# Kernel tuning notes

Measured on AMD Instinct MI355X. Metric: run time of the kernel, lower is better.

Reference implementation:

```python
import jax, jax.numpy as jnp
import numpy as np

N = 50000   # nodes
E = 100000  # edges
C = 256     # in_channels


def setup_inputs() -> dict:
    key = jax.random.key(0)
    k1, k2, k3, k4 = jax.random.split(key, 4)
    x = jax.random.normal(k1, (N, C), dtype=jnp.float32)
    edge_index = jax.random.randint(k2, (2, E), 0, N, dtype=jnp.int32)
    # torch nn.Linear default init ~ U(-1/sqrt(C), 1/sqrt(C)); exact dist irrelevant for correctness
    bound = 1.0 / np.sqrt(C)
    W = jax.random.uniform(k3, (C, C), minval=-bound, maxval=bound, dtype=jnp.float32)
    b = jax.random.uniform(k4, (C,), minval=-bound, maxval=bound, dtype=jnp.float32)
    return {"x": x, "edge_index": edge_index, "W": W, "b": b}


def _scatter_mean_with_self_loops(xt, edge_index, n):
    # edge_index_sl = [edges ; self-loops]
    ar = jnp.arange(n, dtype=edge_index.dtype)
    src = jnp.concatenate([edge_index[0], ar])  # [E+N]
    dst = jnp.concatenate([edge_index[1], ar])  # [E+N]
    gathered = xt[src]                           # [E+N, C]
    sums = jax.ops.segment_sum(gathered, dst, num_segments=n)
    cnt = jax.ops.segment_sum(jnp.ones_like(dst, dtype=xt.dtype), dst, num_segments=n)
    # every node has a self-loop so cnt >= 1; guard anyway
    return sums / jnp.maximum(cnt, 1.0)[:, None]


def _merge_edges(edge_index, n):
    # Sequential greedy edge merge, faithful to the Python loop, as a lax.scan.
    remaining0 = jnp.ones((n,), dtype=jnp.int32)
    discarded0 = jnp.zeros((n,), dtype=jnp.int32).at[edge_index[0]].set(1)

    def step(carry, st):
        rem, disc = carry
        s, t = st[0], st[1]
        cond = (rem[s] == 1) & (rem[t] == 1) & (disc[t] == 1) & (s != t)
        rem = rem.at[s].set(jnp.where(cond, 0, rem[s]))
        disc = disc.at[t].set(jnp.where(cond, 0, disc[t]))
        return (rem, disc), None

    (remaining, _), _ = jax.lax.scan(step, (remaining0, discarded0), edge_index.T)
    return remaining  # int32 0/1 mask, 1 = kept node


def reference(x, edge_index, W, b):
    n = x.shape[0]
    xt = x @ W.T + b                                   # self.trans(x)
    h = _scatter_mean_with_self_loops(xt, edge_index, n)  # [N, C]
    mask = _merge_edges(edge_index, n)                 # nodes_remaining
    # Original returns h[mask == 1] (data-dependent shape). For jit-compatibility
    # we return h with dropped rows zeroed, plus the mask; compaction is a
    # trivial post-processing gather.
    out = h * mask.astype(h.dtype)[:, None]
    return out, mask
```

## Files before the change

### kernel.cpp

```cpp
#include <hip/hip_runtime.h>
#include <hip/hip_bf16.h>

#define C_DIM 256

#define MBLK 64
#define MTHR 1024
#define MT_TOT (MBLK * MTHR)
#define MEPT 2
#define EPOCH0 2000u
#define MAXR 1900
#define GROWS 128

typedef __attribute__((ext_vector_type(8))) short bf16x8;
typedef __attribute__((ext_vector_type(4))) float f32x4;

__device__ __forceinline__ unsigned short f32_to_bf16(float f) {
    __hip_bfloat16 h = __float2bfloat16(f);
    return __builtin_bit_cast(unsigned short, h);
}
__device__ __forceinline__ float bf16_to_f32(unsigned short u) {
    unsigned v = ((unsigned)u) << 16;
    return __builtin_bit_cast(float, v);
}
__device__ __forceinline__ unsigned ld_ag(const unsigned* p) {
    return __hip_atomic_load(p, __ATOMIC_RELAXED, __HIP_MEMORY_SCOPE_AGENT);
}
__device__ __forceinline__ unsigned long long ld_ag8(const unsigned* p) {
    return __hip_atomic_load((const unsigned long long*)p, __ATOMIC_RELAXED, __HIP_MEMORY_SCOPE_AGENT);
}

__global__ __launch_bounds__(256) void prep(const float* __restrict__ W,
                                            unsigned short* __restrict__ W_bf,
                                            const int* __restrict__ esrc,
                                            const int* __restrict__ edst,
                                            unsigned char* __restrict__ disc0,
                                            int* __restrict__ cnt,
                                            unsigned short* __restrict__ slots,
                                            int E) {
    int tid = blockIdx.x * blockDim.x + threadIdx.x;
    int T = gridDim.x * blockDim.x;
    for (int i = tid; i < C_DIM * C_DIM; i += T) W_bf[i] = f32_to_bf16(W[i]);
    for (int e = tid; e < E; e += T) {
        int s = esrc[e], t = edst[e];
        disc0[s] = 1;
        int pos = atomicAdd(&cnt[t], 1);
        if (pos < 32) slots[(size_t)t * 32 + pos] = (unsigned short)s;
    }
}

__global__ __launch_bounds__(1024) void fused_kernel(
    const float* __restrict__ X, const unsigned short* __restrict__ W_bf,
    const float* __restrict__ bias, float* __restrict__ out,
    const int* __restrict__ cnt, const unsigned short* __restrict__ slots,
    const int* __restrict__ esrc, const int* __restrict__ edst,
    const unsigned char* __restrict__ disc0,
    unsigned* __restrict__ mins, unsigned* __restrict__ bar,
    float* __restrict__ remf, int E, int N) {
    __shared__ unsigned short Xs[GROWS][264];

    if (blockIdx.x >= MBLK) {
        const int i0 = (int)(blockIdx.x - MBLK) * GROWS;
        const int tid = threadIdx.x;
        const int w = tid >> 6, l = tid & 63;

        for (int nn = 0; nn < 8; ++nn) {
            int lrow = w * 8 + nn;
            int node = i0 + lrow;
            float4 s = make_float4(0.f, 0.f, 0.f, 0.f);
            if (node < N) {
                s = *(const float4*)&X[(size_t)node * C_DIM + l * 4];
                int deg = cnt[node];
                int dl = deg > 32 ? 32 : deg;
                const unsigned short* sl = slots + (size_t)node * 32;
                unsigned long long sl4 = *(const unsigned long long*)sl;
                int dl4 = dl > 4 ? 4 : dl;
#pragma unroll 4
                for (int j = 0; j < dl4; ++j) {
                    int src = (int)((sl4 >> (16 * j)) & 0xFFFFull);
                    float4 v = *(const float4*)&X[(size_t)src * C_DIM + l * 4];
                    s.x += v.x; s.y += v.y; s.z += v.z; s.w += v.w;
                }
                for (int j = 4; j < dl; ++j) {
                    int src = sl[j];
                    float4 v = *(const float4*)&X[(size_t)src * C_DIM + l * 4];
                    s.x += v.x; s.y += v.y; s.z += v.z; s.w += v.w;
                }
                float inv = 1.f / (float)(deg + 1);
                s.x *= inv; s.y *= inv; s.z *= inv; s.w *= inv;
            }
            ushort4 u;
            u.x = f32_to_bf16(s.x); u.y = f32_to_bf16(s.y);
            u.z = f32_to_bf16(s.z); u.w = f32_to_bf16(s.w);
            *(ushort4*)&Xs[lrow][l * 4] = u;
        }
        __syncthreads();

        const int wr = w >> 2, wc = w & 3;
        const int lr = l & 15, lkq = l >> 4;
        f32x4 acc[2][4] = {};
#pragma unroll
        for (int r = 0; r < 8; ++r) {
            bf16x8 a[2];
#pragma unroll
            for (int ai = 0; ai < 2; ++ai)
                a[ai] = *(const bf16x8*)&Xs[wr * 32 + ai * 16 + lr][r * 32 + lkq * 8];
#pragma unroll
            for (int bj = 0; bj < 4; ++bj) {
                int col = wc * 64 + bj * 16 + lr;
                bf16x8 b = *(const bf16x8*)(W_bf + (size_t)col * C_DIM + r * 32 + lkq * 8);
#pragma unroll
                for (int ai = 0; ai < 2; ++ai)
                    acc[ai][bj] = __builtin_amdgcn_mfma_f32_16x16x32_bf16(a[ai], b, acc[ai][bj], 0, 0, 0);
            }
        }

#pragma unroll
        for (int bj = 0; bj < 4; ++bj) {
            int col = wc * 64 + bj * 16 + lr;
            float bv = bias[col];
#pragma unroll
            for (int ai = 0; ai < 2; ++ai) {
#pragma unroll
                for (int q = 0; q < 4; ++q) {
                    int row = i0 + wr * 32 + ai * 16 + lkq * 4 + q;
                    if (row < N)
                        out[(size_t)row * C_DIM + col] = acc[ai][bj][q] + bv;
                }
            }
        }
        return;
    }

    __shared__ unsigned ldsAny;
    __shared__ unsigned ldsChg;
    const int gtid = blockIdx.x * MTHR + threadIdx.x;
    const int tid = threadIdx.x;

    int es[MEPT], ts[MEPT];
    bool cand[MEPT], fire[MEPT];
#pragma unroll
    for (int i = 0; i < MEPT; ++i) {
        int e = gtid + i * MT_TOT;
        es[i] = 0; ts[i] = 0; cand[i] = false;
        if (e < E) {
            es[i] = esrc[e]; ts[i] = edst[e];
            cand[i] = (es[i] != ts[i]) && (disc0[ts[i]] != 0);
        }
        fire[i] = cand[i];
    }
    if (tid == 0) ldsAny = 0;
    __syncthreads();

    unsigned gen = 0;
    unsigned prevAny = 1;
    int r = 0;
    while (true) {
        if (r > 0) {
            unsigned tagP = (EPOCH0 - (unsigned)(r - 1)) << 20;
            const unsigned* pm = mins + (size_t)((r - 1) & 1) * 2 * N;
            bool anych = false;
#pragma unroll
            for (int i = 0; i < MEPT; ++i) {
                if (cand[i]) {
                    unsigned e = (unsigned)(gtid + i * MT_TOT);
                    unsigned va = ld_ag(&pm[2 * es[i]]);
                    unsigned long long p8 = ld_ag8(&pm[2 * ts[i]]);
                    unsigned vb = (unsigned)p8;
                    unsigned vc = (unsigned)(p8 >> 32);
                    bool blk = ((va - tagP) < e) | ((vb - tagP) < e) | ((vc - tagP) < e);
                    bool nf = !blk;
                    anych |= (nf != fire[i]);
                    fire[i] = nf;
                }
            }
            if (anych) ldsAny = 1;
        }
        {
            unsigned tagC = (EPOCH0 - (unsigned)r) << 20;
            unsigned* cm = mins + (size_t)(r & 1) * 2 * N;
#pragma unroll
            for (int i = 0; i < MEPT; ++i) {
                if (fire[i]) {
                    unsigned e = (unsigned)(gtid + i * MT_TOT);
                    atomicMin(&cm[2 * es[i]], tagC | e);
                    atomicMin(&cm[2 * ts[i] + 1], tagC | e);
                }
            }
        }
        __syncthreads();
        unsigned blockAny = (r == 0) ? 1u : ldsAny;
        ++gen;

        if (tid == 0) {
            unsigned bits = (r == 0) ? 3u
                          : ((blockAny << (r & 1)) | (prevAny << ((r - 1) & 1)));
            __hip_atomic_store(&bar[blockIdx.x * 16], (gen << 2) | bits,
                               __ATOMIC_RELEASE, __HIP_MEMORY_SCOPE_AGENT);
            ldsAny = 0;
        }
        if (tid < 64) {
            unsigned target = gen << 2;
            unsigned v;
            for (;;) {
                v = __hip_atomic_load(&bar[tid * 16], __ATOMIC_RELAXED, __HIP_MEMORY_SCOPE_AGENT);
                if ((int)(v - target) >= 0) break;
                __builtin_amdgcn_s_sleep(1);
            }
            __threadfence();
            unsigned chg = ((v >> (r & 1)) & 1) ? 1u : 0u;
            unsigned long long bl = __ballot(chg != 0);
            if (tid == 0) ldsChg = (bl != 0ull) ? 1u : 0u;
        }
        __syncthreads();
        unsigned globalChg = ldsChg;
        prevAny = blockAny;
        if (r > 0 && globalChg == 0) break;
        if (r >= MAXR) break;
        ++r;
    }

    unsigned tagF = (EPOCH0 - (unsigned)r) << 20;
    const unsigned* fm = mins + (size_t)(r & 1) * 2 * N;
    for (int x = gtid; x < N; x += MT_TOT) {
        unsigned v = ld_ag(&fm[2 * x]);
        remf[x] = ((v - tagF) < (1u << 20)) ? 0.f : 1.f;
    }
}

__global__ __launch_bounds__(256) void mask_zero(const float* __restrict__ remf,
                                                 float* __restrict__ out, int N) {
    int wv = threadIdx.x >> 6, lane = threadIdx.x & 63;
    int node = blockIdx.x * 4 + wv;
    if (node >= N) return;
    float m = remf[node];
    if (lane == 0) out[(size_t)N * C_DIM + node] = m;
    if (m == 0.f) {
        float4 z = make_float4(0.f, 0.f, 0.f, 0.f);
        *(float4*)&out[(size_t)node * C_DIM + lane * 4] = z;
    }
}

extern "C" void kernel_launch(void* const* d_in, const int* in_sizes, int n_in,
                              void* d_out, int out_size, void* d_ws, size_t ws_size,
                              hipStream_t stream) {
    const float* X = (const float*)d_in[0];
    const int* EI = (const int*)d_in[1];
    const float* W = (const float*)d_in[2];
    const float* bias = (const float*)d_in[3];
    const int N = in_sizes[0] / C_DIM;
    const int E = in_sizes[1] / 2;
    const int* esrc = EI;
    const int* edst = EI + E;
    float* out = (float*)d_out;

    char* p = (char*)d_ws;
    auto take = [&](size_t bytes) {
        char* q = p;
        p += (bytes + 255) & ~(size_t)255;
        return q;
    };
    unsigned short* W_bf  = (unsigned short*)take((size_t)C_DIM * C_DIM * 2);
    int* cnt              = (int*)take((size_t)N * 4);
    unsigned short* slots = (unsigned short*)take((size_t)N * 32 * 2);
    unsigned* mins        = (unsigned*)take((size_t)4 * N * 4);
    float* remf           = (float*)take((size_t)N * 4);
    unsigned char* disc0  = (unsigned char*)take((size_t)N);
    unsigned* bar         = (unsigned*)take((size_t)MBLK * 16 * 4);
    (void)ws_size; (void)n_in; (void)out_size;

    hipMemsetAsync(disc0, 0, N, stream);
    hipMemsetAsync(cnt, 0, (size_t)N * 4, stream);

    prep<<<256, 256, 0, stream>>>(W, W_bf, esrc, edst, disc0, cnt, slots, E);

    int nGemm = (N + GROWS - 1) / GROWS;
    fused_kernel<<<MBLK + nGemm, MTHR, 0, stream>>>(X, W_bf, bias, out, cnt, slots,
                                                    esrc, edst, disc0,
                                                    mins, bar, remf, E, N);

    mask_zero<<<(N + 3) / 4, 256, 0, stream>>>(remf, out, N);
}
```

Measured before the change: 248.0 us.

## Fuse mask-zero into merge blocks and convert W on the fly

Removes the separate mask_zero launch. The merge-phase blocks now wait on a global done counter that GEMM blocks increment, then write the mask and zero dropped rows themselves. The W fp32-to-bf16 pre-conversion in prep is dropped, and GEMM blocks load fp32 W and convert it inside the MFMA loop. The two memsets are merged into one. The cost is redundant W conversion in every GEMM block and doubled W read bandwidth. The cross-block spin-wait also depends on all GEMM blocks making progress while the merge blocks stay resident.

Result: slower. 330.9 us (+33.5%).

```diff
diff --git a/kernel.cpp b/kernel.cpp
--- a/kernel.cpp
+++ b/kernel.cpp
@@ -18,10 +18,6 @@
     __hip_bfloat16 h = __float2bfloat16(f);
     return __builtin_bit_cast(unsigned short, h);
 }
-__device__ __forceinline__ float bf16_to_f32(unsigned short u) {
-    unsigned v = ((unsigned)u) << 16;
-    return __builtin_bit_cast(float, v);
-}
 __device__ __forceinline__ unsigned ld_ag(const unsigned* p) {
     return __hip_atomic_load(p, __ATOMIC_RELAXED, __HIP_MEMORY_SCOPE_AGENT);
 }
@@ -29,9 +25,7 @@
     return __hip_atomic_load((const unsigned long long*)p, __ATOMIC_RELAXED, __HIP_MEMORY_SCOPE_AGENT);
 }
 
-__global__ __launch_bounds__(256) void prep(const float* __restrict__ W,
-                                            unsigned short* __restrict__ W_bf,
-                                            const int* __restrict__ esrc,
+__global__ __launch_bounds__(256) void prep(const int* __restrict__ esrc,
                                             const int* __restrict__ edst,
                                             unsigned char* __restrict__ disc0,
                                             int* __restrict__ cnt,
@@ -39,7 +33,6 @@
                                             int E) {
     int tid = blockIdx.x * blockDim.x + threadIdx.x;
     int T = gridDim.x * blockDim.x;
-    for (int i = tid; i < C_DIM * C_DIM; i += T) W_bf[i] = f32_to_bf16(W[i]);
     for (int e = tid; e < E; e += T) {
         int s = esrc[e], t = edst[e];
         disc0[s] = 1;
@@ -49,13 +42,13 @@
 }
 
 __global__ __launch_bounds__(1024) void fused_kernel(
-    const float* __restrict__ X, const unsigned short* __restrict__ W_bf,
+    const float* __restrict__ X, const float* __restrict__ W,
     const float* __restrict__ bias, float* __restrict__ out,
     const int* __restrict__ cnt, const unsigned short* __restrict__ slots,
     const int* __restrict__ esrc, const int* __restrict__ edst,
     const unsigned char* __restrict__ disc0,
     unsigned* __restrict__ mins, unsigned* __restrict__ bar,
-    float* __restrict__ remf, int E, int N) {
+    unsigned* __restrict__ done, int nGemm, int E, int N) {
     __shared__ unsigned short Xs[GROWS][264];
 
     if (blockIdx.x >= MBLK) {
@@ -107,7 +100,14 @@
 #pragma unroll
             for (int bj = 0; bj < 4; ++bj) {
                 int col = wc * 64 + bj * 16 + lr;
-                bf16x8 b = *(const bf16x8*)(W_bf + (size_t)col * C_DIM + r * 32 + lkq * 8);
+                const float* wrow = W + (size_t)col * C_DIM + r * 32 + lkq * 8;
+                float4 w0 = *(const float4*)wrow;
+                float4 w1 = *(const float4*)(wrow + 4);
+                bf16x8 b;
+                b[0] = (short)f32_to_bf16(w0.x); b[1] = (short)f32_to_bf16(w0.y);
+                b[2] = (short)f32_to_bf16(w0.z); b[3] = (short)f32_to_bf16(w0.w);
+                b[4] = (short)f32_to_bf16(w1.x); b[5] = (short)f32_to_bf16(w1.y);
+                b[6] = (short)f32_to_bf16(w1.z); b[7] = (short)f32_to_bf16(w1.w);
 #pragma unroll
                 for (int ai = 0; ai < 2; ++ai)
                     acc[ai][bj] = __builtin_amdgcn_mfma_f32_16x16x32_bf16(a[ai], b, acc[ai][bj], 0, 0, 0);
@@ -127,6 +127,12 @@
                         out[(size_t)row * C_DIM + col] = acc[ai][bj][q] + bv;
                 }
             }
+        }
+
+        __syncthreads();
+        if (threadIdx.x == 0) {
+            __threadfence();
+            __hip_atomic_fetch_add(done, 1u, __ATOMIC_RELEASE, __HIP_MEMORY_SCOPE_AGENT);
         }
         return;
     }
@@ -219,24 +225,25 @@
         ++r;
     }
 
+    if (tid == 0) {
+        while (__hip_atomic_load(done, __ATOMIC_ACQUIRE, __HIP_MEMORY_SCOPE_AGENT) < (unsigned)nGemm)
+            __builtin_amdgcn_s_sleep(2);
+    }
+    __syncthreads();
+    __threadfence();
+
     unsigned tagF = (EPOCH0 - (unsigned)r) << 20;
     const unsigned* fm = mins + (size_t)(r & 1) * 2 * N;
-    for (int x = gtid; x < N; x += MT_TOT) {
+    const int gwave = gtid >> 6;
+    const int lane = tid & 63;
+    for (int x = gwave; x < N; x += MT_TOT >> 6) {
         unsigned v = ld_ag(&fm[2 * x]);
-        remf[x] = ((v - tagF) < (1u << 20)) ? 0.f : 1.f;
-    }
-}
-
-__global__ __launch_bounds__(256) void mask_zero(const float* __restrict__ remf,
-                                                 float* __restrict__ out, int N) {
-    int wv = threadIdx.x >> 6, lane = threadIdx.x & 63;
-    int node = blockIdx.x * 4 + wv;
-    if (node >= N) return;
-    float m = remf[node];
-    if (lane == 0) out[(size_t)N * C_DIM + node] = m;
-    if (m == 0.f) {
-        float4 z = make_float4(0.f, 0.f, 0.f, 0.f);
-        *(float4*)&out[(size_t)node * C_DIM + lane * 4] = z;
+        float m = ((v - tagF) < (1u << 20)) ? 0.f : 1.f;
+        if (lane == 0) out[(size_t)N * C_DIM + x] = m;
+        if (m == 0.f) {
+            float4 z = make_float4(0.f, 0.f, 0.f, 0.f);
+            *(float4*)&out[(size_t)x * C_DIM + lane * 4] = z;
+        }
     }
 }
 
@@ -259,24 +266,22 @@
         p += (bytes + 255) & ~(size_t)255;
         return q;
     };
-    unsigned short* W_bf  = (unsigned short*)take((size_t)C_DIM * C_DIM * 2);
-    int* cnt              = (int*)take((size_t)N * 4);
     unsigned short* slots = (unsigned short*)take((size_t)N * 32 * 2);
     unsigned* mins        = (unsigned*)take((size_t)4 * N * 4);
-    float* remf           = (float*)take((size_t)N * 4);
-    unsigned char* disc0  = (unsigned char*)take((size_t)N);
     unsigned* bar         = (unsigned*)take((size_t)MBLK * 16 * 4);
+    size_t zsz = (size_t)N * 4 + (size_t)N + 16;
+    char* zbase = take(zsz);
+    int* cnt             = (int*)zbase;
+    unsigned char* disc0 = (unsigned char*)(zbase + (size_t)N * 4);
+    unsigned* done       = (unsigned*)(zbase + (size_t)N * 4 + (((size_t)N + 7) & ~(size_t)7));
     (void)ws_size; (void)n_in; (void)out_size;
 
-    hipMemsetAsync(disc0, 0, N, stream);
-    hipMemsetAsync(cnt, 0, (size_t)N * 4, stream);
-
-    prep<<<256, 256, 0, stream>>>(W, W_bf, esrc, edst, disc0, cnt, slots, E);
+    hipMemsetAsync(zbase, 0, zsz, stream);
+
+    prep<<<256, 256, 0, stream>>>(esrc, edst, disc0, cnt, slots, E);
 
     int nGemm = (N + GROWS - 1) / GROWS;
-    fused_kernel<<<MBLK + nGemm, MTHR, 0, stream>>>(X, W_bf, bias, out, cnt, slots,
+    fused_kernel<<<MBLK + nGemm, MTHR, 0, stream>>>(X, W, bias, out, cnt, slots,
                                                     esrc, edst, disc0,
-                                                    mins, bar, remf, E, N);
-
-    mask_zero<<<(N + 3) / 4, 256, 0, stream>>>(remf, out, N);
-}
+                                                    mins, bar, done, nGemm, E, N);
+}
```
